# Performance work log

Measured on AMD Instinct MI355X. Metric: run time of the kernel, lower is better.

## Reference

```python
import jax, jax.numpy as jnp
import numpy as np


def setup_inputs() -> dict:
    key = jax.random.key(0)
    k1, k2 = jax.random.split(key)
    embeddings = jax.random.normal(k1, (32, 512, 1024), dtype=jnp.float32)
    aspect = jax.random.normal(k2, (32, 1024), dtype=jnp.float32)
    return {"embeddings": embeddings, "aspect": aspect}


def reference(embeddings, aspect):
    # go_backwards=False, so no sequence reversal.
    # L2-normalize embeddings per token and aspect per sample.
    e = embeddings / jnp.linalg.norm(embeddings, axis=2, keepdims=True)
    a = aspect / jnp.linalg.norm(aspect, axis=1, keepdims=True)
    # NaN-mask (zero-norm rows produce NaN after division).
    e = jnp.where(jnp.isnan(e), jnp.zeros_like(e), e)
    a = jnp.where(jnp.isnan(a), jnp.zeros_like(a), a)
    # Circulant matrix: circ[b, i, j] = a[b, (j - i) mod D]
    # (matches the TF scatter_nd construction M[i, (i+k)%D] = a[k]).
    D = e.shape[-1]
    r = jnp.arange(D)
    idx = (r[None, :] - r[:, None]) % D  # [D, D]
    circ = a[:, idx]  # [B, D, D]
    # matmul(e, circ, transpose_b=True): out[b,s,i] = sum_j e[b,s,j] * circ[b,i,j]
    return jnp.einsum('bsd,bid->bsi', e, circ)
```

## Files before the change

kernel.cpp:

```cpp
#include <hip/hip_runtime.h>
#include <hip/hip_bf16.h>

typedef __attribute__((ext_vector_type(8))) short bf16x8;
typedef __attribute__((ext_vector_type(4))) float f32x4;

#define NB 32
#define NS 512
#define ND 1024

__device__ __forceinline__ unsigned short f2bf(float f) {
  unsigned int u = __float_as_uint(f);
  u = (u + 0x7FFFu + ((u >> 16) & 1u)) >> 16;
  return (unsigned short)u;
}

__global__ __launch_bounds__(256)
void enormbf_fused_kernel(const float* __restrict__ emb,
                          unsigned short* __restrict__ eN,
                          const float* __restrict__ aspect,
                          unsigned short* __restrict__ a_n) {
  int wave = threadIdx.x >> 6, lane = threadIdx.x & 63;
  size_t row = (size_t)blockIdx.x * 4 + wave;
  const float4* p = (const float4*)(emb + row * ND);
  float4 v[4];
  float s = 0.f;
#pragma unroll
  for (int j = 0; j < 4; ++j) {
    v[j] = p[lane + 64 * j];
    s += v[j].x * v[j].x + v[j].y * v[j].y + v[j].z * v[j].z + v[j].w * v[j].w;
  }
#pragma unroll
  for (int off = 32; off >= 1; off >>= 1) s += __shfl_xor(s, off);
  float inv = (s > 0.f) ? (1.f / sqrtf(s)) : 0.f;
  ushort4* o = (ushort4*)(eN + row * ND);
#pragma unroll
  for (int j = 0; j < 4; ++j) {
    ushort4 u;
    u.x = f2bf(v[j].x * inv); u.y = f2bf(v[j].y * inv);
    u.z = f2bf(v[j].z * inv); u.w = f2bf(v[j].w * inv);
    o[lane + 64 * j] = u;
  }

  if (blockIdx.x < NB) {
    int b = blockIdx.x;
    int t = threadIdx.x;
    const float4* pa = (const float4*)(aspect + (size_t)b * ND);
    float4 va = pa[t];
    float sa = va.x * va.x + va.y * va.y + va.z * va.z + va.w * va.w;
#pragma unroll
    for (int off = 32; off >= 1; off >>= 1) sa += __shfl_down(sa, off);
    __shared__ float red[4];
    if ((t & 63) == 0) red[t >> 6] = sa;
    __syncthreads();
    float tot = red[0] + red[1] + red[2] + red[3];
    float inva = (tot > 0.f) ? (1.f / sqrtf(tot)) : 0.f;
    ushort4 u;
    u.x = f2bf(va.x * inva); u.y = f2bf(va.y * inva);
    u.z = f2bf(va.z * inva); u.w = f2bf(va.w * inva);
    ((ushort4*)(a_n + (size_t)b * ND))[t] = u;
  }
}

__global__ __launch_bounds__(256, 2)
void corr_gemm8_kernel(const unsigned short* __restrict__ eN,
                       const unsigned short* __restrict__ a_n,
                       float* __restrict__ out) {
  __shared__ __align__(16) unsigned short Alds[3 * 8192];
  __shared__ __align__(16) unsigned short copies[8 * 1288];

  const int b = blockIdx.x, mt = blockIdx.y, nt = blockIdx.z;
  const int n0 = nt * 256, m0 = mt * 128;
  const int tid = threadIdx.x;

  const int lane = tid & 63, wn = tid >> 6;
  const int q = lane >> 4, l16 = lane & 15;
  const int mx = l16 & 7;
  const int s00 = (q ^ mx) * 8;
  const int s01 = ((4 + q) ^ mx) * 8;
  const int arow = l16 * 64;

  const int pB = (8 - mx) & 7;
  const unsigned short* Bp = copies + pB * 1287 + (256 + 8 * q - wn * 64 - l16);

  const unsigned short* gstage =
      eN + ((size_t)b * NS + m0 + (tid >> 3)) * ND + (size_t)(((tid & 7) ^ ((tid >> 3) & 7)) * 8);
  char* ldsAbase = (char*)Alds;

  unsigned short av[40];
  {
    const unsigned short* an = a_n + (size_t)b * ND;
    const int p = tid & 7;
    const int x0 = (tid >> 3) * 40;
    const int base = (768 - n0 + p) & 1023;
#pragma unroll
    for (int j = 0; j < 40; ++j) av[j] = an[(base + x0 + j) & 1023];
  }

#pragma unroll
  for (int j = 0; j < 4; ++j)
    __builtin_amdgcn_global_load_lds(
        (const __attribute__((address_space(1))) void*)(gstage + (size_t)j * 32 * ND),
        (__attribute__((address_space(3))) void*)(ldsAbase + (size_t)tid * 16 + j * 4096),
        16, 0, 0);
#pragma unroll
  for (int j = 0; j < 4; ++j)
    __builtin_amdgcn_global_load_lds(
        (const __attribute__((address_space(1))) void*)(gstage + (size_t)j * 32 * ND + 64),
        (__attribute__((address_space(3))) void*)(ldsAbase + 16384 + (size_t)tid * 16 + j * 4096),
        16, 0, 0);

  {
    const int p = tid & 7;
    const int x0 = (tid >> 3) * 40;
#pragma unroll
    for (int j = 0; j < 40; ++j) copies[p * 1288 + x0 + j] = av[j];
  }

  f32x4 acc[8][4];
#pragma unroll
  for (int i = 0; i < 8; ++i)
#pragma unroll
    for (int j = 0; j < 4; ++j)
      acc[i][j] = (f32x4){0.f, 0.f, 0.f, 0.f};

  asm volatile("s_waitcnt lgkmcnt(0)" ::: "memory");
  __builtin_amdgcn_sched_barrier(0);
  __builtin_amdgcn_s_barrier();
  asm volatile("s_waitcnt vmcnt(4)" ::: "memory");
  __builtin_amdgcn_sched_barrier(0);
  __builtin_amdgcn_s_barrier();

  bf16x8 a0[4], a1[4], bfr[4][2];

#define ISSUE_A(DST, BASE, PHN)                                          \
  do {                                                                   \
    DST[0] = *(const bf16x8*)&(BASE)[arow + (PHN) * 2048 + s00];         \
    DST[1] = *(const bf16x8*)&(BASE)[arow + (PHN) * 2048 + s01];         \
    DST[2] = *(const bf16x8*)&(BASE)[arow + (PHN) * 2048 + 1024 + s00];  \
    DST[3] = *(const bf16x8*)&(BASE)[arow + (PHN) * 2048 + 1024 + s01];  \
  } while (0)

#define STAGE4(SLOT, KTT)                                                              \
  do {                                                                                 \
    const unsigned short* sg_ = gstage + (size_t)(KTT) * 64;                           \
    char* dl_ = ldsAbase + (SLOT) * 16384 + (size_t)tid * 16;                          \
    _Pragma("unroll")                                                                  \
    for (int j = 0; j < 4; ++j)                                                        \
      __builtin_amdgcn_global_load_lds(                                                \
          (const __attribute__((address_space(1))) void*)(sg_ + (size_t)j * 32 * ND),  \
          (__attribute__((address_space(3))) void*)(dl_ + j * 4096), 16, 0, 0);        \
  } while (0)

#define LOAD_B(KTT)                                                 \
  do {                                                              \
    const unsigned short* Bt = Bp + (KTT) * 64;                     \
    _Pragma("unroll")                                               \
    for (int n = 0; n < 4; ++n) {                                   \
      bfr[n][0] = *(const bf16x8*)(Bt - n * 16);                    \
      bfr[n][1] = *(const bf16x8*)(Bt + 32 - n * 16);               \
    }                                                               \
  } while (0)

#define MFMA_PH(PH, CS)                                                                       \
  do {                                                                                        \
    __builtin_amdgcn_s_setprio(1);                                                            \
    _Pragma("unroll")                                                                         \
    for (int n = 0; n < 4; ++n) {                                                             \
      acc[2*(PH)][n]   = __builtin_amdgcn_mfma_f32_16x16x32_bf16(CS[0], bfr[n][0], acc[2*(PH)][n],   0, 0, 0); \
      acc[2*(PH)][n]   = __builtin_amdgcn_mfma_f32_16x16x32_bf16(CS[1], bfr[n][1], acc[2*(PH)][n],   0, 0, 0); \
      acc[2*(PH)+1][n] = __builtin_amdgcn_mfma_f32_16x16x32_bf16(CS[2], bfr[n][0], acc[2*(PH)+1][n], 0, 0, 0); \
      acc[2*(PH)+1][n] = __builtin_amdgcn_mfma_f32_16x16x32_bf16(CS[3], bfr[n][1], acc[2*(PH)+1][n], 0, 0, 0); \
    }                                                                                         \
    __builtin_amdgcn_s_setprio(0);                                                            \
  } while (0)

  int c0 = 0, c1 = 1, c2 = 2;

#pragma unroll 1
  for (int kt = 0; kt < 16; ++kt) {
    const unsigned short* At = Alds + c0 * 8192;

    if (kt + 2 < 16) STAGE4(c2, kt + 2);

    ISSUE_A(a0, At, 0);
    LOAD_B(kt);
    ISSUE_A(a1, At, 1);
    asm volatile("s_waitcnt lgkmcnt(4)" ::: "memory");
    __builtin_amdgcn_sched_barrier(0);
    MFMA_PH(0, a0);

    ISSUE_A(a0, At, 2);
    asm volatile("s_waitcnt lgkmcnt(4)" ::: "memory");
    __builtin_amdgcn_sched_barrier(0);
    MFMA_PH(1, a1);

    ISSUE_A(a1, At, 3);
    asm volatile("s_waitcnt lgkmcnt(4)" ::: "memory");
    __builtin_amdgcn_sched_barrier(0);
    MFMA_PH(2, a0);

    asm volatile("s_waitcnt lgkmcnt(0)" ::: "memory");
    __builtin_amdgcn_sched_barrier(0);
    MFMA_PH(3, a1);

    if (kt < 14) {
      asm volatile("s_waitcnt vmcnt(4)" ::: "memory");
    } else if (kt == 14) {
      asm volatile("s_waitcnt vmcnt(0)" ::: "memory");
    }
    __builtin_amdgcn_sched_barrier(0);
    __builtin_amdgcn_s_barrier();

    int tmp = c0; c0 = c1; c1 = c2; c2 = tmp;
  }
#undef MFMA_PH
#undef LOAD_B
#undef STAGE4
#undef ISSUE_A

  float* outB = out + ((size_t)b * NS + m0) * ND + n0;
#pragma unroll
  for (int i = 0; i < 8; ++i) {
#pragma unroll
    for (int rg = 0; rg < 4; ++rg) {
      int r = i * 16 + q * 4 + rg;
      float* orow = outB + (size_t)r * ND + wn * 64 + l16;
#pragma unroll
      for (int n = 0; n < 4; ++n)
        orow[n * 16] = acc[i][n][rg];
    }
  }
}

__global__ void anorm_kernel(const float* __restrict__ aspect,
                             unsigned short* __restrict__ a_n) {
  int b = blockIdx.x;
  int t = threadIdx.x;
  const float4* p = (const float4*)(aspect + (size_t)b * ND);
  float4 v = p[t];
  float s = v.x * v.x + v.y * v.y + v.z * v.z + v.w * v.w;
#pragma unroll
  for (int off = 32; off >= 1; off >>= 1) s += __shfl_down(s, off);
  __shared__ float red[4];
  if ((t & 63) == 0) red[t >> 6] = s;
  __syncthreads();
  float tot = red[0] + red[1] + red[2] + red[3];
  float inv = (tot > 0.f) ? (1.f / sqrtf(tot)) : 0.f;
  ushort4 u;
  u.x = f2bf(v.x * inv); u.y = f2bf(v.y * inv);
  u.z = f2bf(v.z * inv); u.w = f2bf(v.w * inv);
  ((ushort4*)(a_n + (size_t)b * ND))[t] = u;
}

__global__ void enorm_kernel(const float* __restrict__ emb,
                             float* __restrict__ inv_norm) {
  int wave = threadIdx.x >> 6;
  int lane = threadIdx.x & 63;
  int row = blockIdx.x * 4 + wave;
  const float4* p = (const float4*)(emb + (size_t)row * ND);
  float s = 0.f;
#pragma unroll
  for (int j = 0; j < 4; ++j) {
    float4 v = p[lane + 64 * j];
    s += v.x * v.x + v.y * v.y + v.z * v.z + v.w * v.w;
  }
#pragma unroll
  for (int off = 32; off >= 1; off >>= 1) s += __shfl_down(s, off);
  if (lane == 0) inv_norm[row] = (s > 0.f) ? (1.f / sqrtf(s)) : 0.f;
}

__global__ __launch_bounds__(256)
void corr_gemm_kernel(const float* __restrict__ emb,
                      const float* __restrict__ inv_norm,
                      const unsigned short* __restrict__ a_n,
                      float* __restrict__ out) {
  __shared__ unsigned short copies[8][2056];
  __shared__ unsigned short Atile[128][40];

  const int nt = blockIdx.x, mt = blockIdx.y, b = blockIdx.z;
  const int n0 = nt * 128, m0 = mt * 128;
  const int t = threadIdx.x;

  {
    const unsigned short* an = a_n + (size_t)b * ND;
    int p = t & 7;
    int x0 = (t >> 3) * 64;
#pragma unroll
    for (int j = 0; j < 64; j += 4) {
      ushort4 u;
      u.x = an[(x0 + j + 0 + p) & 1023];
      u.y = an[(x0 + j + 1 + p) & 1023];
      u.z = an[(x0 + j + 2 + p) & 1023];
      u.w = an[(x0 + j + 3 + p) & 1023];
      *(ushort4*)&copies[p][x0 + j] = u;
    }
  }

  const int ar = t >> 3;
  const int ac = (t & 7) * 4;
  float invn[4];
#pragma unroll
  for (int w = 0; w < 4; ++w)
    invn[w] = inv_norm[b * NS + m0 + ar + 32 * w];

  const int lane = t & 63;
  const int wv = t >> 6;
  const int wm = wv >> 1, wn = wv & 1;
  const int q = lane >> 4, l16 = lane & 15;

  f32x4 acc[4][4];
#pragma unroll
  for (int i = 0; i < 4; ++i)
#pragma unroll
    for (int j = 0; j < 4; ++j)
      acc[i][j] = (f32x4){0.f, 0.f, 0.f, 0.f};

  const float* embB = emb + ((size_t)b * NS + m0) * ND;

  for (int k0 = 0; k0 < ND; k0 += 32) {
    __syncthreads();
#pragma unroll
    for (int w = 0; w < 4; ++w) {
      int r = ar + 32 * w;
      float4 v = *(const float4*)(embB + (size_t)r * ND + k0 + ac);
      float in = invn[w];
      ushort4 u;
      u.x = f2bf(v.x * in); u.y = f2bf(v.y * in);
      u.z = f2bf(v.z * in); u.w = f2bf(v.w * in);
      *(ushort4*)&Atile[r][ac] = u;
    }
    __syncthreads();

    bf16x8 af[4], bfr[4];
#pragma unroll
    for (int r = 0; r < 4; ++r) {
      int m = wm * 64 + r * 16 + l16;
      af[r] = *(const bf16x8*)&Atile[m][q * 8];
    }
#pragma unroll
    for (int r = 0; r < 4; ++r) {
      int ng = n0 + wn * 64 + r * 16 + l16;
      int e0 = k0 + 8 * q - ng + 1024;
      int p = e0 & 7;
      bfr[r] = *(const bf16x8*)&copies[p][e0 - p];
    }
#pragma unroll
    for (int i = 0; i < 4; ++i)
#pragma unroll
      for (int j = 0; j < 4; ++j)
        acc[i][j] = __builtin_amdgcn_mfma_f32_16x16x32_bf16(af[i], bfr[j], acc[i][j], 0, 0, 0);
  }

  float* outB = out + ((size_t)b * NS + m0) * ND + n0;
#pragma unroll
  for (int i = 0; i < 4; ++i) {
#pragma unroll
    for (int rg = 0; rg < 4; ++rg) {
      int s = wm * 64 + i * 16 + q * 4 + rg;
      float* orow = outB + (size_t)s * ND + wn * 64 + l16;
#pragma unroll
      for (int j = 0; j < 4; ++j)
        orow[j * 16] = acc[i][j][rg];
    }
  }
}

extern "C" void kernel_launch(void* const* d_in, const int* in_sizes, int n_in,
                              void* d_out, int out_size, void* d_ws, size_t ws_size,
                              hipStream_t stream) {
  const float* emb = (const float*)d_in[0];
  const float* aspect = (const float*)d_in[1];
  float* out = (float*)d_out;

  const size_t need = 65536 + (size_t)NB * NS * ND * 2;

  if (ws_size >= need) {
    unsigned short* a_n = (unsigned short*)d_ws;
    unsigned short* eN = (unsigned short*)((char*)d_ws + 65536);
    enormbf_fused_kernel<<<4096, 256, 0, stream>>>(emb, eN, aspect, a_n);
    corr_gemm8_kernel<<<dim3(NB, 4, 4), 256, 0, stream>>>(eN, a_n, out);
  } else {
    float* inv_norm = (float*)d_ws;
    unsigned short* a_n = (unsigned short*)((char*)d_ws + 65536);
    enorm_kernel<<<4096, 256, 0, stream>>>(emb, inv_norm);
    anorm_kernel<<<NB, 256, 0, stream>>>(aspect, a_n);
    corr_gemm_kernel<<<dim3(8, 4, NB), 256, 0, stream>>>(emb, inv_norm, a_n, out);
  }
}
```

Before: 136.9 us.

## Halve GEMM M-tile to 64 rows with double-buffered LDS staging

```diff
diff --git a/kernel.cpp b/kernel.cpp
--- a/kernel.cpp
+++ b/kernel.cpp
@@ -61,15 +61,15 @@
   }
 }
 
-__global__ __launch_bounds__(256, 2)
-void corr_gemm8_kernel(const unsigned short* __restrict__ eN,
+__global__ __launch_bounds__(256)
+void corr_gemm9_kernel(const unsigned short* __restrict__ eN,
                        const unsigned short* __restrict__ a_n,
                        float* __restrict__ out) {
-  __shared__ __align__(16) unsigned short Alds[3 * 8192];
+  __shared__ __align__(16) unsigned short Alds[2 * 4096];
   __shared__ __align__(16) unsigned short copies[8 * 1288];
 
   const int b = blockIdx.x, mt = blockIdx.y, nt = blockIdx.z;
-  const int n0 = nt * 256, m0 = mt * 128;
+  const int n0 = nt * 256, m0 = mt * 64;
   const int tid = threadIdx.x;
 
   const int lane = tid & 63, wn = tid >> 6;
@@ -97,17 +97,11 @@
   }
 
 #pragma unroll
-  for (int j = 0; j < 4; ++j)
+  for (int j = 0; j < 2; ++j)
     __builtin_amdgcn_global_load_lds(
         (const __attribute__((address_space(1))) void*)(gstage + (size_t)j * 32 * ND),
         (__attribute__((address_space(3))) void*)(ldsAbase + (size_t)tid * 16 + j * 4096),
         16, 0, 0);
-#pragma unroll
-  for (int j = 0; j < 4; ++j)
-    __builtin_amdgcn_global_load_lds(
-        (const __attribute__((address_space(1))) void*)(gstage + (size_t)j * 32 * ND + 64),
-        (__attribute__((address_space(3))) void*)(ldsAbase + 16384 + (size_t)tid * 16 + j * 4096),
-        16, 0, 0);
 
   {
     const int p = tid & 7;
@@ -116,9 +110,9 @@
     for (int j = 0; j < 40; ++j) copies[p * 1288 + x0 + j] = av[j];
   }
 
-  f32x4 acc[8][4];
-#pragma unroll
-  for (int i = 0; i < 8; ++i)
+  f32x4 acc[4][4];
+#pragma unroll
+  for (int i = 0; i < 4; ++i)
 #pragma unroll
     for (int j = 0; j < 4; ++j)
       acc[i][j] = (f32x4){0.f, 0.f, 0.f, 0.f};
@@ -126,101 +120,69 @@
   asm volatile("s_waitcnt lgkmcnt(0)" ::: "memory");
   __builtin_amdgcn_sched_barrier(0);
   __builtin_amdgcn_s_barrier();
-  asm volatile("s_waitcnt vmcnt(4)" ::: "memory");
+  asm volatile("s_waitcnt vmcnt(0)" ::: "memory");
   __builtin_amdgcn_sched_barrier(0);
   __builtin_amdgcn_s_barrier();
 
-  bf16x8 a0[4], a1[4], bfr[4][2];
-
-#define ISSUE_A(DST, BASE, PHN)                                          \
-  do {                                                                   \
-    DST[0] = *(const bf16x8*)&(BASE)[arow + (PHN) * 2048 + s00];         \
-    DST[1] = *(const bf16x8*)&(BASE)[arow + (PHN) * 2048 + s01];         \
-    DST[2] = *(const bf16x8*)&(BASE)[arow + (PHN) * 2048 + 1024 + s00];  \
-    DST[3] = *(const bf16x8*)&(BASE)[arow + (PHN) * 2048 + 1024 + s01];  \
-  } while (0)
-
-#define STAGE4(SLOT, KTT)                                                              \
+  bf16x8 a0[4], a1[4], b0[4], b1[4];
+
+#define STAGE2(SLOT, KTT)                                                              \
   do {                                                                                 \
     const unsigned short* sg_ = gstage + (size_t)(KTT) * 64;                           \
-    char* dl_ = ldsAbase + (SLOT) * 16384 + (size_t)tid * 16;                          \
+    char* dl_ = ldsAbase + (SLOT) * 8192 + (size_t)tid * 16;                           \
     _Pragma("unroll")                                                                  \
-    for (int j = 0; j < 4; ++j)                                                        \
+    for (int j = 0; j < 2; ++j)                                                        \
       __builtin_amdgcn_global_load_lds(                                                \
           (const __attribute__((address_space(1))) void*)(sg_ + (size_t)j * 32 * ND),  \
           (__attribute__((address_space(3))) void*)(dl_ + j * 4096), 16, 0, 0);        \
   } while (0)
 
-#define LOAD_B(KTT)                                                 \
-  do {                                                              \
-    const unsigned short* Bt = Bp + (KTT) * 64;                     \
-    _Pragma("unroll")                                               \
-    for (int n = 0; n < 4; ++n) {                                   \
-      bfr[n][0] = *(const bf16x8*)(Bt - n * 16);                    \
-      bfr[n][1] = *(const bf16x8*)(Bt + 32 - n * 16);               \
-    }                                                               \
+#define MFMA16(AR, BR)                                                                 \
+  do {                                                                                 \
+    __builtin_amdgcn_s_setprio(1);                                                     \
+    _Pragma("unroll")                                                                  \
+    for (int n = 0; n < 4; ++n) {                                                      \
+      _Pragma("unroll")                                                                \
+      for (int r = 0; r < 4; ++r)                                                      \
+        acc[r][n] = __builtin_amdgcn_mfma_f32_16x16x32_bf16(AR[r], BR[n], acc[r][n], 0, 0, 0); \
+    }                                                                                  \
+    __builtin_amdgcn_s_setprio(0);                                                     \
   } while (0)
-
-#define MFMA_PH(PH, CS)                                                                       \
-  do {                                                                                        \
-    __builtin_amdgcn_s_setprio(1);                                                            \
-    _Pragma("unroll")                                                                         \
-    for (int n = 0; n < 4; ++n) {                                                             \
-      acc[2*(PH)][n]   = __builtin_amdgcn_mfma_f32_16x16x32_bf16(CS[0], bfr[n][0], acc[2*(PH)][n],   0, 0, 0); \
-      acc[2*(PH)][n]   = __builtin_amdgcn_mfma_f32_16x16x32_bf16(CS[1], bfr[n][1], acc[2*(PH)][n],   0, 0, 0); \
-      acc[2*(PH)+1][n] = __builtin_amdgcn_mfma_f32_16x16x32_bf16(CS[2], bfr[n][0], acc[2*(PH)+1][n], 0, 0, 0); \
-      acc[2*(PH)+1][n] = __builtin_amdgcn_mfma_f32_16x16x32_bf16(CS[3], bfr[n][1], acc[2*(PH)+1][n], 0, 0, 0); \
-    }                                                                                         \
-    __builtin_amdgcn_s_setprio(0);                                                            \
-  } while (0)
-
-  int c0 = 0, c1 = 1, c2 = 2;
 
 #pragma unroll 1
   for (int kt = 0; kt < 16; ++kt) {
-    const unsigned short* At = Alds + c0 * 8192;
-
-    if (kt + 2 < 16) STAGE4(c2, kt + 2);
-
-    ISSUE_A(a0, At, 0);
-    LOAD_B(kt);
-    ISSUE_A(a1, At, 1);
-    asm volatile("s_waitcnt lgkmcnt(4)" ::: "memory");
+    const unsigned short* At = Alds + (kt & 1) * 4096;
+
+    if (kt < 15) STAGE2((kt & 1) ^ 1, kt + 1);
+
+    const unsigned short* Bt = Bp + kt * 64;
+#pragma unroll
+    for (int r = 0; r < 4; ++r) a0[r] = *(const bf16x8*)&At[arow + r * 1024 + s00];
+#pragma unroll
+    for (int n = 0; n < 4; ++n) b0[n] = *(const bf16x8*)(Bt - n * 16);
+#pragma unroll
+    for (int r = 0; r < 4; ++r) a1[r] = *(const bf16x8*)&At[arow + r * 1024 + s01];
+#pragma unroll
+    for (int n = 0; n < 4; ++n) b1[n] = *(const bf16x8*)(Bt + 32 - n * 16);
+
+    asm volatile("s_waitcnt lgkmcnt(8)" ::: "memory");
     __builtin_amdgcn_sched_barrier(0);
-    MFMA_PH(0, a0);
-
-    ISSUE_A(a0, At, 2);
-    asm volatile("s_waitcnt lgkmcnt(4)" ::: "memory");
-    __builtin_amdgcn_sched_barrier(0);
-    MFMA_PH(1, a1);
-
-    ISSUE_A(a1, At, 3);
-    asm volatile("s_waitcnt lgkmcnt(4)" ::: "memory");
-    __builtin_amdgcn_sched_barrier(0);
-    MFMA_PH(2, a0);
+    MFMA16(a0, b0);
 
     asm volatile("s_waitcnt lgkmcnt(0)" ::: "memory");
     __builtin_amdgcn_sched_barrier(0);
-    MFMA_PH(3, a1);
-
-    if (kt < 14) {
-      asm volatile("s_waitcnt vmcnt(4)" ::: "memory");
-    } else if (kt == 14) {
-      asm volatile("s_waitcnt vmcnt(0)" ::: "memory");
-    }
+    MFMA16(a1, b1);
+
+    asm volatile("s_waitcnt vmcnt(0)" ::: "memory");
     __builtin_amdgcn_sched_barrier(0);
     __builtin_amdgcn_s_barrier();
-
-    int tmp = c0; c0 = c1; c1 = c2; c2 = tmp;
-  }
-#undef MFMA_PH
-#undef LOAD_B
-#undef STAGE4
-#undef ISSUE_A
+  }
+#undef MFMA16
+#undef STAGE2
 
   float* outB = out + ((size_t)b * NS + m0) * ND + n0;
 #pragma unroll
-  for (int i = 0; i < 8; ++i) {
+  for (int i = 0; i < 4; ++i) {
 #pragma unroll
     for (int rg = 0; rg < 4; ++rg) {
       int r = i * 16 + q * 4 + rg;
@@ -378,7 +340,7 @@
     unsigned short* a_n = (unsigned short*)d_ws;
     unsigned short* eN = (unsigned short*)((char*)d_ws + 65536);
     enormbf_fused_kernel<<<4096, 256, 0, stream>>>(emb, eN, aspect, a_n);
-    corr_gemm8_kernel<<<dim3(NB, 4, 4), 256, 0, stream>>>(eN, a_n, out);
+    corr_gemm9_kernel<<<dim3(NB, 8, 4), 256, 0, stream>>>(eN, a_n, out);
   } else {
     float* inv_norm = (float*)d_ws;
     unsigned short* a_n = (unsigned short*)((char*)d_ws + 65536);
```

After: 145.7 us. 6.4% more time.

## Precompute shifted aspect copies in global memory and read B fragments directly

Applied to the files above, without the earlier changes.

```diff
diff --git a/kernel.cpp b/kernel.cpp
--- a/kernel.cpp
+++ b/kernel.cpp
@@ -15,10 +15,8 @@
 }
 
 __global__ __launch_bounds__(256)
-void enormbf_fused_kernel(const float* __restrict__ emb,
-                          unsigned short* __restrict__ eN,
-                          const float* __restrict__ aspect,
-                          unsigned short* __restrict__ a_n) {
+void enormbf_kernel2(const float* __restrict__ emb,
+                     unsigned short* __restrict__ eN) {
   int wave = threadIdx.x >> 6, lane = threadIdx.x & 63;
   size_t row = (size_t)blockIdx.x * 4 + wave;
   const float4* p = (const float4*)(emb + row * ND);
@@ -40,33 +38,46 @@
     u.z = f2bf(v[j].z * inv); u.w = f2bf(v[j].w * inv);
     o[lane + 64 * j] = u;
   }
-
-  if (blockIdx.x < NB) {
-    int b = blockIdx.x;
-    int t = threadIdx.x;
-    const float4* pa = (const float4*)(aspect + (size_t)b * ND);
-    float4 va = pa[t];
-    float sa = va.x * va.x + va.y * va.y + va.z * va.z + va.w * va.w;
-#pragma unroll
-    for (int off = 32; off >= 1; off >>= 1) sa += __shfl_down(sa, off);
-    __shared__ float red[4];
-    if ((t & 63) == 0) red[t >> 6] = sa;
-    __syncthreads();
-    float tot = red[0] + red[1] + red[2] + red[3];
-    float inva = (tot > 0.f) ? (1.f / sqrtf(tot)) : 0.f;
+}
+
+__global__ void anorm8_kernel(const float* __restrict__ aspect,
+                              unsigned short* __restrict__ a_n8) {
+  int b = blockIdx.x;
+  int t = threadIdx.x;
+  __shared__ float red[4];
+  __shared__ unsigned short sm[1024];
+  const float4* pa = (const float4*)(aspect + (size_t)b * ND);
+  float4 v = pa[t];
+  float s = v.x * v.x + v.y * v.y + v.z * v.z + v.w * v.w;
+#pragma unroll
+  for (int off = 32; off >= 1; off >>= 1) s += __shfl_down(s, off);
+  if ((t & 63) == 0) red[t >> 6] = s;
+  __syncthreads();
+  float tot = red[0] + red[1] + red[2] + red[3];
+  float inv = (tot > 0.f) ? (1.f / sqrtf(tot)) : 0.f;
+  sm[t * 4 + 0] = f2bf(v.x * inv);
+  sm[t * 4 + 1] = f2bf(v.y * inv);
+  sm[t * 4 + 2] = f2bf(v.z * inv);
+  sm[t * 4 + 3] = f2bf(v.w * inv);
+  __syncthreads();
+  unsigned short* dst = a_n8 + (size_t)b * 16384;
+#pragma unroll
+  for (int p = 0; p < 8; ++p) {
     ushort4 u;
-    u.x = f2bf(va.x * inva); u.y = f2bf(va.y * inva);
-    u.z = f2bf(va.z * inva); u.w = f2bf(va.w * inva);
-    ((ushort4*)(a_n + (size_t)b * ND))[t] = u;
+    u.x = sm[(t * 4 + 0 + p) & 1023];
+    u.y = sm[(t * 4 + 1 + p) & 1023];
+    u.z = sm[(t * 4 + 2 + p) & 1023];
+    u.w = sm[(t * 4 + 3 + p) & 1023];
+    *(ushort4*)(dst + p * 2048 + t * 4) = u;
+    *(ushort4*)(dst + p * 2048 + 1024 + t * 4) = u;
   }
 }
 
 __global__ __launch_bounds__(256, 2)
-void corr_gemm8_kernel(const unsigned short* __restrict__ eN,
-                       const unsigned short* __restrict__ a_n,
-                       float* __restrict__ out) {
+void corr_gemm10_kernel(const unsigned short* __restrict__ eN,
+                        const unsigned short* __restrict__ a_n8,
+                        float* __restrict__ out) {
   __shared__ __align__(16) unsigned short Alds[3 * 8192];
-  __shared__ __align__(16) unsigned short copies[8 * 1288];
 
   const int b = blockIdx.x, mt = blockIdx.y, nt = blockIdx.z;
   const int n0 = nt * 256, m0 = mt * 128;
@@ -80,55 +91,19 @@
   const int arow = l16 * 64;
 
   const int pB = (8 - mx) & 7;
-  const unsigned short* Bp = copies + pB * 1287 + (256 + 8 * q - wn * 64 - l16);
+  const int G0 = 1024 + 8 * q - wn * 64 - l16 - n0;
+  const unsigned short* Bbase = a_n8 + (size_t)b * 16384 + pB * 2048 + (G0 - pB);
 
   const unsigned short* gstage =
       eN + ((size_t)b * NS + m0 + (tid >> 3)) * ND + (size_t)(((tid & 7) ^ ((tid >> 3) & 7)) * 8);
   char* ldsAbase = (char*)Alds;
 
-  unsigned short av[40];
-  {
-    const unsigned short* an = a_n + (size_t)b * ND;
-    const int p = tid & 7;
-    const int x0 = (tid >> 3) * 40;
-    const int base = (768 - n0 + p) & 1023;
-#pragma unroll
-    for (int j = 0; j < 40; ++j) av[j] = an[(base + x0 + j) & 1023];
-  }
-
-#pragma unroll
-  for (int j = 0; j < 4; ++j)
-    __builtin_amdgcn_global_load_lds(
-        (const __attribute__((address_space(1))) void*)(gstage + (size_t)j * 32 * ND),
-        (__attribute__((address_space(3))) void*)(ldsAbase + (size_t)tid * 16 + j * 4096),
-        16, 0, 0);
-#pragma unroll
-  for (int j = 0; j < 4; ++j)
-    __builtin_amdgcn_global_load_lds(
-        (const __attribute__((address_space(1))) void*)(gstage + (size_t)j * 32 * ND + 64),
-        (__attribute__((address_space(3))) void*)(ldsAbase + 16384 + (size_t)tid * 16 + j * 4096),
-        16, 0, 0);
-
-  {
-    const int p = tid & 7;
-    const int x0 = (tid >> 3) * 40;
-#pragma unroll
-    for (int j = 0; j < 40; ++j) copies[p * 1288 + x0 + j] = av[j];
-  }
-
   f32x4 acc[8][4];
 #pragma unroll
   for (int i = 0; i < 8; ++i)
 #pragma unroll
     for (int j = 0; j < 4; ++j)
       acc[i][j] = (f32x4){0.f, 0.f, 0.f, 0.f};
-
-  asm volatile("s_waitcnt lgkmcnt(0)" ::: "memory");
-  __builtin_amdgcn_sched_barrier(0);
-  __builtin_amdgcn_s_barrier();
-  asm volatile("s_waitcnt vmcnt(4)" ::: "memory");
-  __builtin_amdgcn_sched_barrier(0);
-  __builtin_amdgcn_s_barrier();
 
   bf16x8 a0[4], a1[4], bfr[4][2];
 
@@ -151,9 +126,9 @@
           (__attribute__((address_space(3))) void*)(dl_ + j * 4096), 16, 0, 0);        \
   } while (0)
 
-#define LOAD_B(KTT)                                                 \
+#define LOADB(KTT)                                                  \
   do {                                                              \
-    const unsigned short* Bt = Bp + (KTT) * 64;                     \
+    const unsigned short* Bt = Bbase + (KTT) * 64;                  \
     _Pragma("unroll")                                               \
     for (int n = 0; n < 4; ++n) {                                   \
       bfr[n][0] = *(const bf16x8*)(Bt - n * 16);                    \
@@ -174,17 +149,33 @@
     __builtin_amdgcn_s_setprio(0);                                                            \
   } while (0)
 
+  STAGE4(0, 0);
+  STAGE4(1, 1);
+  asm volatile("s_waitcnt vmcnt(4)" ::: "memory");
+  __builtin_amdgcn_sched_barrier(0);
+  __builtin_amdgcn_s_barrier();
+
   int c0 = 0, c1 = 1, c2 = 2;
 
 #pragma unroll 1
   for (int kt = 0; kt < 16; ++kt) {
     const unsigned short* At = Alds + c0 * 8192;
 
-    if (kt + 2 < 16) STAGE4(c2, kt + 2);
+    LOADB(kt);
+    __builtin_amdgcn_sched_barrier(0);
+    if (kt < 14) STAGE4(c2, kt + 2);
+    __builtin_amdgcn_sched_barrier(0);
 
     ISSUE_A(a0, At, 0);
-    LOAD_B(kt);
     ISSUE_A(a1, At, 1);
+
+    if (kt < 14) {
+      asm volatile("s_waitcnt vmcnt(4)" ::: "memory");
+    } else {
+      asm volatile("s_waitcnt vmcnt(0)" ::: "memory");
+    }
+    __builtin_amdgcn_sched_barrier(0);
+
     asm volatile("s_waitcnt lgkmcnt(4)" ::: "memory");
     __builtin_amdgcn_sched_barrier(0);
     MFMA_PH(0, a0);
@@ -203,18 +194,12 @@
     __builtin_amdgcn_sched_barrier(0);
     MFMA_PH(3, a1);
 
-    if (kt < 14) {
-      asm volatile("s_waitcnt vmcnt(4)" ::: "memory");
-    } else if (kt == 14) {
-      asm volatile("s_waitcnt vmcnt(0)" ::: "memory");
-    }
-    __builtin_amdgcn_sched_barrier(0);
     __builtin_amdgcn_s_barrier();
 
     int tmp = c0; c0 = c1; c1 = c2; c2 = tmp;
   }
 #undef MFMA_PH
-#undef LOAD_B
+#undef LOADB
 #undef STAGE4
 #undef ISSUE_A
 
@@ -252,6 +237,134 @@
   ((ushort4*)(a_n + (size_t)b * ND))[t] = u;
 }
 
+__global__ __launch_bounds__(256)
+void corr_gemm9_kernel(const unsigned short* __restrict__ eN,
+                       const unsigned short* __restrict__ a_n,
+                       float* __restrict__ out) {
+  __shared__ __align__(16) unsigned short Alds[2 * 4096];
+  __shared__ __align__(16) unsigned short copies[8 * 1288];
+
+  const int b = blockIdx.x, mt = blockIdx.y, nt = blockIdx.z;
+  const int n0 = nt * 256, m0 = mt * 64;
+  const int tid = threadIdx.x;
+
+  const int lane = tid & 63, wn = tid >> 6;
+  const int q = lane >> 4, l16 = lane & 15;
+  const int mx = l16 & 7;
+  const int s00 = (q ^ mx) * 8;
+  const int s01 = ((4 + q) ^ mx) * 8;
+  const int arow = l16 * 64;
+
+  const int pB = (8 - mx) & 7;
+  const unsigned short* Bp = copies + pB * 1287 + (256 + 8 * q - wn * 64 - l16);
+
+  const unsigned short* gstage =
+      eN + ((size_t)b * NS + m0 + (tid >> 3)) * ND + (size_t)(((tid & 7) ^ ((tid >> 3) & 7)) * 8);
+  char* ldsAbase = (char*)Alds;
+
+  unsigned short av[40];
+  {
+    const unsigned short* an = a_n + (size_t)b * ND;
+    const int p = tid & 7;
+    const int x0 = (tid >> 3) * 40;
+    const int base = (768 - n0 + p) & 1023;
+#pragma unroll
+    for (int j = 0; j < 40; ++j) av[j] = an[(base + x0 + j) & 1023];
+  }
+
+#pragma unroll
+  for (int j = 0; j < 2; ++j)
+    __builtin_amdgcn_global_load_lds(
+        (const __attribute__((address_space(1))) void*)(gstage + (size_t)j * 32 * ND),
+        (__attribute__((address_space(3))) void*)(ldsAbase + (size_t)tid * 16 + j * 4096),
+        16, 0, 0);
+
+  {
+    const int p = tid & 7;
+    const int x0 = (tid >> 3) * 40;
+#pragma unroll
+    for (int j = 0; j < 40; ++j) copies[p * 1288 + x0 + j] = av[j];
+  }
+
+  f32x4 acc[4][4];
+#pragma unroll
+  for (int i = 0; i < 4; ++i)
+#pragma unroll
+    for (int j = 0; j < 4; ++j)
+      acc[i][j] = (f32x4){0.f, 0.f, 0.f, 0.f};
+
+  asm volatile("s_waitcnt lgkmcnt(0)" ::: "memory");
+  __builtin_amdgcn_sched_barrier(0);
+  __builtin_amdgcn_s_barrier();
+  asm volatile("s_waitcnt vmcnt(0)" ::: "memory");
+  __builtin_amdgcn_sched_barrier(0);
+  __builtin_amdgcn_s_barrier();
+
+  bf16x8 a0[4], a1[4], b0[4], b1[4];
+
+#pragma unroll 1
+  for (int kt = 0; kt < 16; ++kt) {
+    const unsigned short* At = Alds + (kt & 1) * 4096;
+
+    if (kt < 15) {
+      const unsigned short* sg_ = gstage + (size_t)(kt + 1) * 64;
+      char* dl_ = ldsAbase + ((kt & 1) ^ 1) * 8192 + (size_t)tid * 16;
+#pragma unroll
+      for (int j = 0; j < 2; ++j)
+        __builtin_amdgcn_global_load_lds(
+            (const __attribute__((address_space(1))) void*)(sg_ + (size_t)j * 32 * ND),
+            (__attribute__((address_space(3))) void*)(dl_ + j * 4096), 16, 0, 0);
+    }
+
+    const unsigned short* Bt = Bp + kt * 64;
+#pragma unroll
+    for (int r = 0; r < 4; ++r) a0[r] = *(const bf16x8*)&At[arow + r * 1024 + s00];
+#pragma unroll
+    for (int n = 0; n < 4; ++n) b0[n] = *(const bf16x8*)(Bt - n * 16);
+#pragma unroll
+    for (int r = 0; r < 4; ++r) a1[r] = *(const bf16x8*)&At[arow + r * 1024 + s01];
+#pragma unroll
+    for (int n = 0; n < 4; ++n) b1[n] = *(const bf16x8*)(Bt + 32 - n * 16);
+
+    asm volatile("s_waitcnt lgkmcnt(8)" ::: "memory");
+    __builtin_amdgcn_sched_barrier(0);
+    __builtin_amdgcn_s_setprio(1);
+#pragma unroll
+    for (int n = 0; n < 4; ++n)
+#pragma unroll
+      for (int r = 0; r < 4; ++r)
+        acc[r][n] = __builtin_amdgcn_mfma_f32_16x16x32_bf16(a0[r], b0[n], acc[r][n], 0, 0, 0);
+    __builtin_amdgcn_s_setprio(0);
+
+    asm volatile("s_waitcnt lgkmcnt(0)" ::: "memory");
+    __builtin_amdgcn_sched_barrier(0);
+    __builtin_amdgcn_s_setprio(1);
+#pragma unroll
+    for (int n = 0; n < 4; ++n)
+#pragma unroll
+      for (int r = 0; r < 4; ++r)
+        acc[r][n] = __builtin_amdgcn_mfma_f32_16x16x32_bf16(a1[r], b1[n], acc[r][n], 0, 0, 0);
+    __builtin_amdgcn_s_setprio(0);
+
+    asm volatile("s_waitcnt vmcnt(0)" ::: "memory");
+    __builtin_amdgcn_sched_barrier(0);
+    __builtin_amdgcn_s_barrier();
+  }
+
+  float* outB = out + ((size_t)b * NS + m0) * ND + n0;
+#pragma unroll
+  for (int i = 0; i < 4; ++i) {
+#pragma unroll
+    for (int rg = 0; rg < 4; ++rg) {
+      int r = i * 16 + q * 4 + rg;
+      float* orow = outB + (size_t)r * ND + wn * 64 + l16;
+#pragma unroll
+      for (int n = 0; n < 4; ++n)
+        orow[n * 16] = acc[i][n][rg];
+    }
+  }
+}
+
 __global__ void enorm_kernel(const float* __restrict__ emb,
                              float* __restrict__ inv_norm) {
   int wave = threadIdx.x >> 6;
@@ -372,13 +485,22 @@
   const float* aspect = (const float*)d_in[1];
   float* out = (float*)d_out;
 
-  const size_t need = 65536 + (size_t)NB * NS * ND * 2;
-
-  if (ws_size >= need) {
+  const size_t eN_bytes = (size_t)NB * NS * ND * 2;
+  const size_t need10 = 1048576 + eN_bytes;
+  const size_t need9 = 65536 + eN_bytes;
+
+  if (ws_size >= need10) {
+    unsigned short* a_n8 = (unsigned short*)d_ws;
+    unsigned short* eN = (unsigned short*)((char*)d_ws + 1048576);
+    anorm8_kernel<<<NB, 256, 0, stream>>>(aspect, a_n8);
+    enormbf_kernel2<<<4096, 256, 0, stream>>>(emb, eN);
+    corr_gemm10_kernel<<<dim3(NB, 4, 4), 256, 0, stream>>>(eN, a_n8, out);
+  } else if (ws_size >= need9) {
     unsigned short* a_n = (unsigned short*)d_ws;
     unsigned short* eN = (unsigned short*)((char*)d_ws + 65536);
-    enormbf_fused_kernel<<<4096, 256, 0, stream>>>(emb, eN, aspect, a_n);
-    corr_gemm8_kernel<<<dim3(NB, 4, 4), 256, 0, stream>>>(eN, a_n, out);
+    anorm_kernel<<<NB, 256, 0, stream>>>(aspect, a_n);
+    enormbf_kernel2<<<4096, 256, 0, stream>>>(emb, eN);
+    corr_gemm9_kernel<<<dim3(NB, 8, 4), 256, 0, stream>>>(eN, a_n, out);
   } else {
     float* inv_norm = (float*)d_ws;
     unsigned short* a_n = (unsigned short*)((char*)d_ws + 65536);
```

After: 145.5 us. +6.2%, slower.

## Fuse embedding normalization into GEMM by loading fp32 and scaling output rows

Applied to the files above, without the earlier changes.

```diff
diff --git a/kernel.cpp b/kernel.cpp
--- a/kernel.cpp
+++ b/kernel.cpp
@@ -3,6 +3,7 @@
 
 typedef __attribute__((ext_vector_type(8))) short bf16x8;
 typedef __attribute__((ext_vector_type(4))) float f32x4;
+typedef __attribute__((ext_vector_type(4))) unsigned int u32x4;
 
 #define NB 32
 #define NS 512
@@ -14,59 +15,33 @@
   return (unsigned short)u;
 }
 
-__global__ __launch_bounds__(256)
-void enormbf_fused_kernel(const float* __restrict__ emb,
-                          unsigned short* __restrict__ eN,
-                          const float* __restrict__ aspect,
-                          unsigned short* __restrict__ a_n) {
-  int wave = threadIdx.x >> 6, lane = threadIdx.x & 63;
-  size_t row = (size_t)blockIdx.x * 4 + wave;
-  const float4* p = (const float4*)(emb + row * ND);
-  float4 v[4];
-  float s = 0.f;
-#pragma unroll
-  for (int j = 0; j < 4; ++j) {
-    v[j] = p[lane + 64 * j];
-    s += v[j].x * v[j].x + v[j].y * v[j].y + v[j].z * v[j].z + v[j].w * v[j].w;
-  }
-#pragma unroll
-  for (int off = 32; off >= 1; off >>= 1) s += __shfl_xor(s, off);
-  float inv = (s > 0.f) ? (1.f / sqrtf(s)) : 0.f;
-  ushort4* o = (ushort4*)(eN + row * ND);
-#pragma unroll
-  for (int j = 0; j < 4; ++j) {
-    ushort4 u;
-    u.x = f2bf(v[j].x * inv); u.y = f2bf(v[j].y * inv);
-    u.z = f2bf(v[j].z * inv); u.w = f2bf(v[j].w * inv);
-    o[lane + 64 * j] = u;
-  }
-
-  if (blockIdx.x < NB) {
-    int b = blockIdx.x;
-    int t = threadIdx.x;
-    const float4* pa = (const float4*)(aspect + (size_t)b * ND);
-    float4 va = pa[t];
-    float sa = va.x * va.x + va.y * va.y + va.z * va.z + va.w * va.w;
-#pragma unroll
-    for (int off = 32; off >= 1; off >>= 1) sa += __shfl_down(sa, off);
-    __shared__ float red[4];
-    if ((t & 63) == 0) red[t >> 6] = sa;
-    __syncthreads();
-    float tot = red[0] + red[1] + red[2] + red[3];
-    float inva = (tot > 0.f) ? (1.f / sqrtf(tot)) : 0.f;
-    ushort4 u;
-    u.x = f2bf(va.x * inva); u.y = f2bf(va.y * inva);
-    u.z = f2bf(va.z * inva); u.w = f2bf(va.w * inva);
-    ((ushort4*)(a_n + (size_t)b * ND))[t] = u;
-  }
+__global__ void anorm_kernel(const float* __restrict__ aspect,
+                             unsigned short* __restrict__ a_n) {
+  int b = blockIdx.x;
+  int t = threadIdx.x;
+  const float4* p = (const float4*)(aspect + (size_t)b * ND);
+  float4 v = p[t];
+  float s = v.x * v.x + v.y * v.y + v.z * v.z + v.w * v.w;
+#pragma unroll
+  for (int off = 32; off >= 1; off >>= 1) s += __shfl_down(s, off);
+  __shared__ float red[4];
+  if ((t & 63) == 0) red[t >> 6] = s;
+  __syncthreads();
+  float tot = red[0] + red[1] + red[2] + red[3];
+  float inv = (tot > 0.f) ? (1.f / sqrtf(tot)) : 0.f;
+  ushort4 u;
+  u.x = f2bf(v.x * inv); u.y = f2bf(v.y * inv);
+  u.z = f2bf(v.z * inv); u.w = f2bf(v.w * inv);
+  ((ushort4*)(a_n + (size_t)b * ND))[t] = u;
 }
 
 __global__ __launch_bounds__(256, 2)
-void corr_gemm8_kernel(const unsigned short* __restrict__ eN,
-                       const unsigned short* __restrict__ a_n,
-                       float* __restrict__ out) {
-  __shared__ __align__(16) unsigned short Alds[3 * 8192];
+void corr_gemm11_kernel(const float* __restrict__ emb,
+                        const unsigned short* __restrict__ a_n,
+                        float* __restrict__ out) {
+  __shared__ __align__(16) unsigned short Abuf[2][128][64];
   __shared__ __align__(16) unsigned short copies[8 * 1288];
+  __shared__ float invnLDS[128];
 
   const int b = blockIdx.x, mt = blockIdx.y, nt = blockIdx.z;
   const int n0 = nt * 256, m0 = mt * 128;
@@ -77,14 +52,13 @@
   const int mx = l16 & 7;
   const int s00 = (q ^ mx) * 8;
   const int s01 = ((4 + q) ^ mx) * 8;
-  const int arow = l16 * 64;
 
   const int pB = (8 - mx) & 7;
   const unsigned short* Bp = copies + pB * 1287 + (256 + 8 * q - wn * 64 - l16);
 
-  const unsigned short* gstage =
-      eN + ((size_t)b * NS + m0 + (tid >> 3)) * ND + (size_t)(((tid & 7) ^ ((tid >> 3) & 7)) * 8);
-  char* ldsAbase = (char*)Alds;
+  const int r0 = tid >> 3, cw = tid & 7;
+  const int sw = cw ^ (r0 & 7);
+  const float* gA = emb + ((size_t)b * NS + m0 + r0) * ND + cw * 8;
 
   unsigned short av[40];
   {
@@ -96,25 +70,47 @@
     for (int j = 0; j < 40; ++j) av[j] = an[(base + x0 + j) & 1023];
   }
 
-#pragma unroll
-  for (int j = 0; j < 4; ++j)
-    __builtin_amdgcn_global_load_lds(
-        (const __attribute__((address_space(1))) void*)(gstage + (size_t)j * 32 * ND),
-        (__attribute__((address_space(3))) void*)(ldsAbase + (size_t)tid * 16 + j * 4096),
-        16, 0, 0);
-#pragma unroll
-  for (int j = 0; j < 4; ++j)
-    __builtin_amdgcn_global_load_lds(
-        (const __attribute__((address_space(1))) void*)(gstage + (size_t)j * 32 * ND + 64),
-        (__attribute__((address_space(3))) void*)(ldsAbase + 16384 + (size_t)tid * 16 + j * 4096),
-        16, 0, 0);
-
+  float4 g[8];
+  float ss0 = 0.f, ss1 = 0.f, ss2 = 0.f, ss3 = 0.f;
+
+#define LOADG(KTT)                                                       \
+  do {                                                                   \
+    _Pragma("unroll")                                                    \
+    for (int j = 0; j < 4; ++j) {                                        \
+      const float* _p = gA + (size_t)j * 32 * ND + (KTT) * 64;           \
+      g[2 * j] = *(const float4*)_p;                                     \
+      g[2 * j + 1] = *(const float4*)(_p + 4);                           \
+    }                                                                    \
+  } while (0)
+
+#define CVT_WRITE(NBUF)                                                  \
+  do {                                                                   \
+    _Pragma("unroll")                                                    \
+    for (int j = 0; j < 4; ++j) {                                        \
+      float4 va = g[2 * j], vb = g[2 * j + 1];                           \
+      float _s = va.x * va.x + va.y * va.y + va.z * va.z + va.w * va.w   \
+               + vb.x * vb.x + vb.y * vb.y + vb.z * vb.z + vb.w * vb.w;  \
+      if (j == 0) ss0 += _s; else if (j == 1) ss1 += _s;                 \
+      else if (j == 2) ss2 += _s; else ss3 += _s;                        \
+      u32x4 w;                                                           \
+      w[0] = (unsigned)f2bf(va.x) | ((unsigned)f2bf(va.y) << 16);        \
+      w[1] = (unsigned)f2bf(va.z) | ((unsigned)f2bf(va.w) << 16);        \
+      w[2] = (unsigned)f2bf(vb.x) | ((unsigned)f2bf(vb.y) << 16);        \
+      w[3] = (unsigned)f2bf(vb.z) | ((unsigned)f2bf(vb.w) << 16);       \
+      *(u32x4*)&Abuf[NBUF][r0 + 32 * j][sw * 8] = w;                     \
+    }                                                                    \
+  } while (0)
+
+  LOADG(0);
   {
     const int p = tid & 7;
     const int x0 = (tid >> 3) * 40;
 #pragma unroll
     for (int j = 0; j < 40; ++j) copies[p * 1288 + x0 + j] = av[j];
   }
+  CVT_WRITE(0);
+  LOADG(1);
+  __syncthreads();
 
   f32x4 acc[8][4];
 #pragma unroll
@@ -123,32 +119,14 @@
     for (int j = 0; j < 4; ++j)
       acc[i][j] = (f32x4){0.f, 0.f, 0.f, 0.f};
 
-  asm volatile("s_waitcnt lgkmcnt(0)" ::: "memory");
-  __builtin_amdgcn_sched_barrier(0);
-  __builtin_amdgcn_s_barrier();
-  asm volatile("s_waitcnt vmcnt(4)" ::: "memory");
-  __builtin_amdgcn_sched_barrier(0);
-  __builtin_amdgcn_s_barrier();
-
   bf16x8 a0[4], a1[4], bfr[4][2];
 
-#define ISSUE_A(DST, BASE, PHN)                                          \
-  do {                                                                   \
-    DST[0] = *(const bf16x8*)&(BASE)[arow + (PHN) * 2048 + s00];         \
-    DST[1] = *(const bf16x8*)&(BASE)[arow + (PHN) * 2048 + s01];         \
-    DST[2] = *(const bf16x8*)&(BASE)[arow + (PHN) * 2048 + 1024 + s00];  \
-    DST[3] = *(const bf16x8*)&(BASE)[arow + (PHN) * 2048 + 1024 + s01];  \
-  } while (0)
-
-#define STAGE4(SLOT, KTT)                                                              \
-  do {                                                                                 \
-    const unsigned short* sg_ = gstage + (size_t)(KTT) * 64;                           \
-    char* dl_ = ldsAbase + (SLOT) * 16384 + (size_t)tid * 16;                          \
-    _Pragma("unroll")                                                                  \
-    for (int j = 0; j < 4; ++j)                                                        \
-      __builtin_amdgcn_global_load_lds(                                                \
-          (const __attribute__((address_space(1))) void*)(sg_ + (size_t)j * 32 * ND),  \
-          (__attribute__((address_space(3))) void*)(dl_ + j * 4096), 16, 0, 0);        \
+#define ISSUE_A(DST, BASE, PHN)                                             \
+  do {                                                                      \
+    DST[0] = *(const bf16x8*)&(BASE)[(PHN) * 32 + l16][s00];                \
+    DST[1] = *(const bf16x8*)&(BASE)[(PHN) * 32 + l16][s01];                \
+    DST[2] = *(const bf16x8*)&(BASE)[(PHN) * 32 + 16 + l16][s00];           \
+    DST[3] = *(const bf16x8*)&(BASE)[(PHN) * 32 + 16 + l16][s01];           \
   } while (0)
 
 #define LOAD_B(KTT)                                                 \
@@ -174,13 +152,9 @@
     __builtin_amdgcn_s_setprio(0);                                                            \
   } while (0)
 
-  int c0 = 0, c1 = 1, c2 = 2;
-
 #pragma unroll 1
   for (int kt = 0; kt < 16; ++kt) {
-    const unsigned short* At = Alds + c0 * 8192;
-
-    if (kt + 2 < 16) STAGE4(c2, kt + 2);
+    const unsigned short (*At)[64] = Abuf[kt & 1];
 
     ISSUE_A(a0, At, 0);
     LOAD_B(kt);
@@ -203,53 +177,50 @@
     __builtin_amdgcn_sched_barrier(0);
     MFMA_PH(3, a1);
 
-    if (kt < 14) {
-      asm volatile("s_waitcnt vmcnt(4)" ::: "memory");
-    } else if (kt == 14) {
+    if (kt < 15) {
       asm volatile("s_waitcnt vmcnt(0)" ::: "memory");
-    }
-    __builtin_amdgcn_sched_barrier(0);
+      __builtin_amdgcn_sched_barrier(0);
+      CVT_WRITE((kt & 1) ^ 1);
+      if (kt < 14) LOADG(kt + 2);
+      asm volatile("s_waitcnt lgkmcnt(0)" ::: "memory");
+      __builtin_amdgcn_sched_barrier(0);
+    }
     __builtin_amdgcn_s_barrier();
-
-    int tmp = c0; c0 = c1; c1 = c2; c2 = tmp;
   }
 #undef MFMA_PH
 #undef LOAD_B
-#undef STAGE4
 #undef ISSUE_A
 
+#pragma unroll
+  for (int off = 4; off >= 1; off >>= 1) {
+    ss0 += __shfl_xor(ss0, off);
+    ss1 += __shfl_xor(ss1, off);
+    ss2 += __shfl_xor(ss2, off);
+    ss3 += __shfl_xor(ss3, off);
+  }
+  if ((lane & 7) == 0) {
+    invnLDS[r0 +  0] = (ss0 > 0.f) ? (1.f / sqrtf(ss0)) : 0.f;
+    invnLDS[r0 + 32] = (ss1 > 0.f) ? (1.f / sqrtf(ss1)) : 0.f;
+    invnLDS[r0 + 64] = (ss2 > 0.f) ? (1.f / sqrtf(ss2)) : 0.f;
+    invnLDS[r0 + 96] = (ss3 > 0.f) ? (1.f / sqrtf(ss3)) : 0.f;
+  }
+  __syncthreads();
+
   float* outB = out + ((size_t)b * NS + m0) * ND + n0;
 #pragma unroll
   for (int i = 0; i < 8; ++i) {
+    f32x4 iv = *(const f32x4*)&invnLDS[i * 16 + q * 4];
 #pragma unroll
     for (int rg = 0; rg < 4; ++rg) {
       int r = i * 16 + q * 4 + rg;
       float* orow = outB + (size_t)r * ND + wn * 64 + l16;
 #pragma unroll
       for (int n = 0; n < 4; ++n)
-        orow[n * 16] = acc[i][n][rg];
-    }
-  }
-}
-
-__global__ void anorm_kernel(const float* __restrict__ aspect,
-                             unsigned short* __restrict__ a_n) {
-  int b = blockIdx.x;
-  int t = threadIdx.x;
-  const float4* p = (const float4*)(aspect + (size_t)b * ND);
-  float4 v = p[t];
-  float s = v.x * v.x + v.y * v.y + v.z * v.z + v.w * v.w;
-#pragma unroll
-  for (int off = 32; off >= 1; off >>= 1) s += __shfl_down(s, off);
-  __shared__ float red[4];
-  if ((t & 63) == 0) red[t >> 6] = s;
-  __syncthreads();
-  float tot = red[0] + red[1] + red[2] + red[3];
-  float inv = (tot > 0.f) ? (1.f / sqrtf(tot)) : 0.f;
-  ushort4 u;
-  u.x = f2bf(v.x * inv); u.y = f2bf(v.y * inv);
-  u.z = f2bf(v.z * inv); u.w = f2bf(v.w * inv);
-  ((ushort4*)(a_n + (size_t)b * ND))[t] = u;
+        orow[n * 16] = acc[i][n][rg] * iv[rg];
+    }
+  }
+#undef CVT_WRITE
+#undef LOADG
 }
 
 __global__ void enorm_kernel(const float* __restrict__ emb,
@@ -372,13 +343,10 @@
   const float* aspect = (const float*)d_in[1];
   float* out = (float*)d_out;
 
-  const size_t need = 65536 + (size_t)NB * NS * ND * 2;
-
-  if (ws_size >= need) {
+  if (ws_size >= 65536) {
     unsigned short* a_n = (unsigned short*)d_ws;
-    unsigned short* eN = (unsigned short*)((char*)d_ws + 65536);
-    enormbf_fused_kernel<<<4096, 256, 0, stream>>>(emb, eN, aspect, a_n);
-    corr_gemm8_kernel<<<dim3(NB, 4, 4), 256, 0, stream>>>(eN, a_n, out);
+    anorm_kernel<<<NB, 256, 0, stream>>>(aspect, a_n);
+    corr_gemm11_kernel<<<dim3(NB, 4, 4), 256, 0, stream>>>(emb, a_n, out);
   } else {
     float* inv_norm = (float*)d_ws;
     unsigned short* a_n = (unsigned short*)((char*)d_ws + 65536);
```

After: 138.6 us. About the same (+1.2%).
